# Kernel tuning notes

Measured on AMD Instinct MI355X. Metric: run time of the kernel, lower is better.

The kernel has to match this reference:

```python
import jax, jax.numpy as jnp
import numpy as np

N_NODES = 100000
N_EDGES = 1600000
D_IN = 256
D_OUT = 128


def setup_inputs() -> dict:
    key = jax.random.key(0)
    k1, k2, k3, k4, k5 = jax.random.split(key, 5)
    features = jax.random.normal(k1, (N_NODES, D_IN), dtype=jnp.float32)
    # Xavier-uniform init for weight [in, out]
    limit = float(np.sqrt(6.0 / (D_IN + D_OUT)))
    weight = jax.random.uniform(k2, (D_IN, D_OUT), dtype=jnp.float32, minval=-limit, maxval=limit)
    edge_rows = jax.random.randint(k3, (N_EDGES,), 0, N_NODES, dtype=jnp.int32)
    edge_cols = jax.random.randint(k4, (N_EDGES,), 0, N_NODES, dtype=jnp.int32)
    edge_vals = jax.random.uniform(k5, (N_EDGES,), dtype=jnp.float32)
    return {
        "features": features,
        "weight": weight,
        "edge_rows": edge_rows,
        "edge_cols": edge_cols,
        "edge_vals": edge_vals,
    }


def reference(features, weight, edge_rows, edge_cols, edge_vals):
    # support = X @ W : [N, D_OUT]
    support = features @ weight
    # SpMM with COO adjacency: out[i] = sum_{e: row[e]==i} vals[e] * support[col[e]]
    gathered = edge_vals[:, None] * support[edge_cols]        # [E, D_OUT]
    output = jax.ops.segment_sum(gathered, edge_rows, num_segments=N_NODES)
    # active=True -> fused ReLU
    return jax.nn.relu(output)
```

## Files before the change

kernel.cpp:

```cpp
#include <hip/hip_runtime.h>

#define N_NODES 100000
#define N_EDGES 1600000
#define D_IN    256
#define D_OUT   128

typedef __attribute__((ext_vector_type(8))) short short8;
typedef __attribute__((ext_vector_type(4))) float floatx4;

static __device__ __forceinline__ ushort f2bf(float f) {
    union { float f; unsigned u; } v; v.f = f;
    unsigned r = v.u + 0x7fffu + ((v.u >> 16) & 1u);
    return (ushort)(r >> 16);
}

__global__ __launch_bounds__(256) void gcn_gemm_mfma(
    const float* __restrict__ X,
    const float* __restrict__ W,
    ushort* __restrict__ supp)
{
    __shared__ ushort wp[32 * 128 * 8];

    const int tid  = threadIdx.x;
    const int lane = tid & 63;
    const int wid  = tid >> 6;
    const int node0 = blockIdx.x * 128;

#pragma unroll
    for (int i = 0; i < 16; ++i) {
        const int p   = i * 256 + tid;
        const int kg  = p >> 7;
        const int col = p & 127;
        const float* wsrc = W + (size_t)(kg * 8) * D_OUT + col;
        short8 v;
#pragma unroll
        for (int ki = 0; ki < 8; ++ki)
            v[ki] = (short)f2bf(wsrc[(size_t)ki * D_OUT]);
        *(short8*)&wp[(size_t)p * 8] = v;
    }
    __syncthreads();

    const int r0    = node0 + wid * 32;
    const int g     = lane >> 4;
    const int arow0 = r0 + (lane & 15);
    const int arow1 = arow0 + 16;
    const int crow0 = arow0 < N_NODES - 1 ? arow0 : N_NODES - 1;
    const int crow1 = arow1 < N_NODES - 1 ? arow1 : N_NODES - 1;

    const float* xp0 = X + (size_t)crow0 * D_IN + g * 8;
    const float* xp1 = X + (size_t)crow1 * D_IN + g * 8;

    floatx4 acc[2][8];
#pragma unroll
    for (int t = 0; t < 2; ++t)
#pragma unroll
        for (int n = 0; n < 8; ++n)
            acc[t][n] = (floatx4){0.f, 0.f, 0.f, 0.f};

#pragma unroll
    for (int ks = 0; ks < 8; ++ks) {
        const float4 u0 = *(const float4*)(xp0 + ks * 32);
        const float4 u1 = *(const float4*)(xp0 + ks * 32 + 4);
        const float4 u2 = *(const float4*)(xp1 + ks * 32);
        const float4 u3 = *(const float4*)(xp1 + ks * 32 + 4);
        short8 a0, a1;
        a0[0] = (short)f2bf(u0.x); a0[1] = (short)f2bf(u0.y);
        a0[2] = (short)f2bf(u0.z); a0[3] = (short)f2bf(u0.w);
        a0[4] = (short)f2bf(u1.x); a0[5] = (short)f2bf(u1.y);
        a0[6] = (short)f2bf(u1.z); a0[7] = (short)f2bf(u1.w);
        a1[0] = (short)f2bf(u2.x); a1[1] = (short)f2bf(u2.y);
        a1[2] = (short)f2bf(u2.z); a1[3] = (short)f2bf(u2.w);
        a1[4] = (short)f2bf(u3.x); a1[5] = (short)f2bf(u3.y);
        a1[6] = (short)f2bf(u3.z); a1[7] = (short)f2bf(u3.w);

        const int kg = ks * 4 + g;
#pragma unroll
        for (int n = 0; n < 8; ++n) {
            const short8 b = *(const short8*)&wp[(size_t)((kg << 7) + n * 16 + (lane & 15)) * 8];
            acc[0][n] = __builtin_amdgcn_mfma_f32_16x16x32_bf16(a0, b, acc[0][n], 0, 0, 0);
            acc[1][n] = __builtin_amdgcn_mfma_f32_16x16x32_bf16(a1, b, acc[1][n], 0, 0, 0);
        }
    }

#pragma unroll
    for (int t = 0; t < 2; ++t) {
        const int rbase = r0 + t * 16 + (lane >> 4) * 4;
#pragma unroll
        for (int n = 0; n < 8; ++n) {
            const int col = n * 16 + (lane & 15);
#pragma unroll
            for (int i = 0; i < 4; ++i) {
                const int row = rbase + i;
                if (row < N_NODES)
                    supp[(size_t)row * D_OUT + col] = f2bf(acc[t][n][i]);
            }
        }
    }
}

__global__ __launch_bounds__(256) void gcn_hist_kernel(
    const int* __restrict__ rows, int* __restrict__ counts)
{
    int e = blockIdx.x * 256 + threadIdx.x;
    if (e < N_EDGES) atomicAdd(&counts[rows[e]], 1);
}

__global__ __launch_bounds__(256) void gcn_scan1_kernel(
    const int* __restrict__ counts, int* __restrict__ off, int* __restrict__ bsums)
{
    __shared__ int t[256];
    const int tid = threadIdx.x;
    const int i0 = blockIdx.x * 1024 + tid * 4;

    int c0 = 0, c1 = 0, c2 = 0, c3 = 0;
    if (i0 + 3 < N_NODES) {
        int4 v = *(const int4*)&counts[i0];
        c0 = v.x; c1 = v.y; c2 = v.z; c3 = v.w;
    } else {
        if (i0 + 0 < N_NODES) c0 = counts[i0 + 0];
        if (i0 + 1 < N_NODES) c1 = counts[i0 + 1];
        if (i0 + 2 < N_NODES) c2 = counts[i0 + 2];
        if (i0 + 3 < N_NODES) c3 = counts[i0 + 3];
    }
    const int s = c0 + c1 + c2 + c3;
    t[tid] = s;
    __syncthreads();

    for (int d = 1; d < 256; d <<= 1) {
        int x = t[tid];
        int add = (tid >= d) ? t[tid - d] : 0;
        __syncthreads();
        t[tid] = x + add;
        __syncthreads();
    }
    const int excl = t[tid] - s;
    if (tid == 255) bsums[blockIdx.x] = t[255];

    const int e0 = excl;
    const int e1 = e0 + c0;
    const int e2 = e1 + c1;
    const int e3 = e2 + c2;
    if (i0 + 0 < N_NODES) off[i0 + 0] = e0;
    if (i0 + 1 < N_NODES) off[i0 + 1] = e1;
    if (i0 + 2 < N_NODES) off[i0 + 2] = e2;
    if (i0 + 3 < N_NODES) off[i0 + 3] = e3;
}

__global__ __launch_bounds__(128) void gcn_scan2_kernel(int* __restrict__ bsums, int nb)
{
    __shared__ int t[128];
    const int tid = threadIdx.x;
    const int v = (tid < nb) ? bsums[tid] : 0;
    t[tid] = v;
    __syncthreads();
    for (int d = 1; d < 128; d <<= 1) {
        int x = t[tid];
        int add = (tid >= d) ? t[tid - d] : 0;
        __syncthreads();
        t[tid] = x + add;
        __syncthreads();
    }
    if (tid < nb) bsums[tid] = t[tid] - v;
}

__global__ __launch_bounds__(256) void gcn_scan3_kernel(
    const int* __restrict__ bsums, int* __restrict__ off, int* __restrict__ cursor)
{
    int i = blockIdx.x * 256 + threadIdx.x;
    if (i < N_NODES) {
        int o = off[i] + bsums[i >> 10];
        off[i] = o;
        cursor[i] = o;
    }
}

__global__ __launch_bounds__(256) void gcn_scatter_kernel(
    const int* __restrict__ rows, const int* __restrict__ cols,
    const float* __restrict__ vals, int* __restrict__ cursor,
    int2* __restrict__ edges)
{
    int e = blockIdx.x * 256 + threadIdx.x;
    if (e < N_EDGES) {
        int pos = atomicAdd(&cursor[rows[e]], 1);
        edges[pos] = make_int2(cols[e], __float_as_int(vals[e]));
    }
}

__global__ __launch_bounds__(256) void gcn_aggregate_kernel(
    const int* __restrict__ off, const int* __restrict__ ends,
    const int2* __restrict__ edges, const unsigned* __restrict__ supp2,
    float* __restrict__ out)
{
    const int node = blockIdx.x * 4 + (threadIdx.x >> 6);
    if (node >= N_NODES) return;
    const int lane = threadIdx.x & 63;

    const int start = off[node];
    const int end   = ends[node];

    float accx = 0.f, accy = 0.f;

    for (int base = start; base < end; base += 64) {
        int m = end - base;
        if (m > 64) m = 64;
        int2 e = edges[base + (lane < m ? lane : 0)];
        for (int j = 0; j < m; ++j) {
            const int      col = __shfl(e.x, j);
            const float    v   = __int_as_float(__shfl(e.y, j));
            const unsigned s   = supp2[(size_t)col * 64 + lane];
            accx = fmaf(v, __uint_as_float(s << 16), accx);
            accy = fmaf(v, __uint_as_float(s & 0xffff0000u), accy);
        }
    }

    float2 o;
    o.x = accx > 0.f ? accx : 0.f;
    o.y = accy > 0.f ? accy : 0.f;
    ((float2*)out)[(size_t)node * 64 + lane] = o;
}

extern "C" void kernel_launch(void* const* d_in, const int* in_sizes, int n_in,
                              void* d_out, int out_size, void* d_ws, size_t ws_size,
                              hipStream_t stream)
{
    const float* X    = (const float*)d_in[0];
    const float* W    = (const float*)d_in[1];
    const int*   rows = (const int*)  d_in[2];
    const int*   cols = (const int*)  d_in[3];
    const float* vals = (const float*)d_in[4];
    float* out = (float*)d_out;

    char* ws = (char*)d_ws;
    size_t p = 0;
    ushort* supp   = (ushort*)(ws + p); p += (size_t)N_NODES * D_OUT * 2;
    int*    counts = (int*)   (ws + p); p += (size_t)N_NODES * 4;
    int*    off    = (int*)   (ws + p); p += (size_t)N_NODES * 4;
    int*    cursor = (int*)   (ws + p); p += (size_t)N_NODES * 4;
    int*    bsums  = (int*)   (ws + p); p += 512;
    int2*   edges  = (int2*)  (ws + p); p += (size_t)N_EDGES * 8;
    (void)ws_size;

    const int NB = (N_NODES + 1023) / 1024;

    gcn_gemm_mfma<<<(N_NODES + 127) / 128, 256, 0, stream>>>(X, W, supp);

    (void)hipMemsetAsync(counts, 0, (size_t)N_NODES * 4, stream);
    gcn_hist_kernel<<<(N_EDGES + 255) / 256, 256, 0, stream>>>(rows, counts);
    gcn_scan1_kernel<<<NB, 256, 0, stream>>>(counts, off, bsums);
    gcn_scan2_kernel<<<1, 128, 0, stream>>>(bsums, NB);
    gcn_scan3_kernel<<<(N_NODES + 255) / 256, 256, 0, stream>>>(bsums, off, cursor);
    gcn_scatter_kernel<<<(N_EDGES + 255) / 256, 256, 0, stream>>>(rows, cols, vals, cursor, edges);

    gcn_aggregate_kernel<<<(N_NODES + 3) / 4, 256, 0, stream>>>(
        off, cursor, edges, (const unsigned*)supp, out);
}
```

Measured before the change: 480.4 us.

## Bucket edges by 128-row groups and aggregate with shared-memory atomics

Result: slower. 1.645 ms (+242.5%).

```diff
diff --git a/kernel.cpp b/kernel.cpp
--- a/kernel.cpp
+++ b/kernel.cpp
@@ -4,6 +4,11 @@
 #define N_EDGES 1600000
 #define D_IN    256
 #define D_OUT   128
+
+#define BROWS    128
+#define NBUCKETS ((N_NODES + BROWS - 1) / BROWS)
+#define EPB      4096
+#define NPART    ((N_EDGES + EPB - 1) / EPB)
 
 typedef __attribute__((ext_vector_type(8))) short short8;
 typedef __attribute__((ext_vector_type(4))) float floatx4;
@@ -98,30 +103,40 @@
     }
 }
 
-__global__ __launch_bounds__(256) void gcn_hist_kernel(
-    const int* __restrict__ rows, int* __restrict__ counts)
-{
-    int e = blockIdx.x * 256 + threadIdx.x;
-    if (e < N_EDGES) atomicAdd(&counts[rows[e]], 1);
-}
-
-__global__ __launch_bounds__(256) void gcn_scan1_kernel(
-    const int* __restrict__ counts, int* __restrict__ off, int* __restrict__ bsums)
+__global__ __launch_bounds__(256) void gcn_bcount(
+    const int* __restrict__ rows, int* __restrict__ bcount)
+{
+    __shared__ int h[NBUCKETS];
+    const int tid = threadIdx.x;
+    for (int i = tid; i < NBUCKETS; i += 256) h[i] = 0;
+    __syncthreads();
+
+    const int e0 = blockIdx.x * EPB;
+#pragma unroll
+    for (int i = 0; i < EPB / 256; ++i) {
+        const int e = e0 + i * 256 + tid;
+        if (e < N_EDGES) atomicAdd(&h[rows[e] >> 7], 1);
+    }
+    __syncthreads();
+
+    for (int i = tid; i < NBUCKETS; i += 256) {
+        const int c = h[i];
+        if (c) atomicAdd(&bcount[i], c);
+    }
+}
+
+__global__ __launch_bounds__(256) void gcn_bscan(
+    const int* __restrict__ bcount, int* __restrict__ boff, int* __restrict__ gcursor)
 {
     __shared__ int t[256];
     const int tid = threadIdx.x;
-    const int i0 = blockIdx.x * 1024 + tid * 4;
+    const int i0 = tid * 4;
 
     int c0 = 0, c1 = 0, c2 = 0, c3 = 0;
-    if (i0 + 3 < N_NODES) {
-        int4 v = *(const int4*)&counts[i0];
-        c0 = v.x; c1 = v.y; c2 = v.z; c3 = v.w;
-    } else {
-        if (i0 + 0 < N_NODES) c0 = counts[i0 + 0];
-        if (i0 + 1 < N_NODES) c1 = counts[i0 + 1];
-        if (i0 + 2 < N_NODES) c2 = counts[i0 + 2];
-        if (i0 + 3 < N_NODES) c3 = counts[i0 + 3];
-    }
+    if (i0 + 0 < NBUCKETS) c0 = bcount[i0 + 0];
+    if (i0 + 1 < NBUCKETS) c1 = bcount[i0 + 1];
+    if (i0 + 2 < NBUCKETS) c2 = bcount[i0 + 2];
+    if (i0 + 3 < NBUCKETS) c3 = bcount[i0 + 3];
     const int s = c0 + c1 + c2 + c3;
     t[tid] = s;
     __syncthreads();
@@ -134,89 +149,120 @@
         __syncthreads();
     }
     const int excl = t[tid] - s;
-    if (tid == 255) bsums[blockIdx.x] = t[255];
 
     const int e0 = excl;
     const int e1 = e0 + c0;
     const int e2 = e1 + c1;
     const int e3 = e2 + c2;
-    if (i0 + 0 < N_NODES) off[i0 + 0] = e0;
-    if (i0 + 1 < N_NODES) off[i0 + 1] = e1;
-    if (i0 + 2 < N_NODES) off[i0 + 2] = e2;
-    if (i0 + 3 < N_NODES) off[i0 + 3] = e3;
-}
-
-__global__ __launch_bounds__(128) void gcn_scan2_kernel(int* __restrict__ bsums, int nb)
-{
-    __shared__ int t[128];
+    if (i0 + 0 < NBUCKETS) { boff[i0 + 0] = e0; gcursor[i0 + 0] = e0; }
+    if (i0 + 1 < NBUCKETS) { boff[i0 + 1] = e1; gcursor[i0 + 1] = e1; }
+    if (i0 + 2 < NBUCKETS) { boff[i0 + 2] = e2; gcursor[i0 + 2] = e2; }
+    if (i0 + 3 < NBUCKETS) { boff[i0 + 3] = e3; gcursor[i0 + 3] = e3; }
+}
+
+__global__ __launch_bounds__(256) void gcn_bscatter(
+    const int* __restrict__ rows, const int* __restrict__ cols,
+    const float* __restrict__ vals, int* __restrict__ gcursor,
+    int2* __restrict__ edges)
+{
+    __shared__ int h[NBUCKETS];
     const int tid = threadIdx.x;
-    const int v = (tid < nb) ? bsums[tid] : 0;
-    t[tid] = v;
-    __syncthreads();
-    for (int d = 1; d < 128; d <<= 1) {
-        int x = t[tid];
-        int add = (tid >= d) ? t[tid - d] : 0;
-        __syncthreads();
-        t[tid] = x + add;
-        __syncthreads();
-    }
-    if (tid < nb) bsums[tid] = t[tid] - v;
-}
-
-__global__ __launch_bounds__(256) void gcn_scan3_kernel(
-    const int* __restrict__ bsums, int* __restrict__ off, int* __restrict__ cursor)
-{
-    int i = blockIdx.x * 256 + threadIdx.x;
-    if (i < N_NODES) {
-        int o = off[i] + bsums[i >> 10];
-        off[i] = o;
-        cursor[i] = o;
-    }
-}
-
-__global__ __launch_bounds__(256) void gcn_scatter_kernel(
-    const int* __restrict__ rows, const int* __restrict__ cols,
-    const float* __restrict__ vals, int* __restrict__ cursor,
-    int2* __restrict__ edges)
-{
-    int e = blockIdx.x * 256 + threadIdx.x;
-    if (e < N_EDGES) {
-        int pos = atomicAdd(&cursor[rows[e]], 1);
-        edges[pos] = make_int2(cols[e], __float_as_int(vals[e]));
-    }
-}
-
-__global__ __launch_bounds__(256) void gcn_aggregate_kernel(
-    const int* __restrict__ off, const int* __restrict__ ends,
+    for (int i = tid; i < NBUCKETS; i += 256) h[i] = 0;
+    __syncthreads();
+
+    const int e0 = blockIdx.x * EPB;
+    int bk[EPB / 256];
+    int rl[EPB / 256];
+#pragma unroll
+    for (int i = 0; i < EPB / 256; ++i) {
+        const int e = e0 + i * 256 + tid;
+        bk[i] = -1;
+        if (e < N_EDGES) {
+            const int r = rows[e];
+            bk[i] = r >> 7;
+            rl[i] = r & 127;
+            atomicAdd(&h[bk[i]], 1);
+        }
+    }
+    __syncthreads();
+
+    for (int i = tid; i < NBUCKETS; i += 256) {
+        const int c = h[i];
+        h[i] = c ? atomicAdd(&gcursor[i], c) : 0;
+    }
+    __syncthreads();
+
+#pragma unroll
+    for (int i = 0; i < EPB / 256; ++i) {
+        if (bk[i] >= 0) {
+            const int e = e0 + i * 256 + tid;
+            const int pos = atomicAdd(&h[bk[i]], 1);
+            edges[pos] = make_int2((rl[i] << 17) | cols[e], __float_as_int(vals[e]));
+        }
+    }
+}
+
+__global__ __launch_bounds__(256) void gcn_baggregate(
+    const int* __restrict__ boff, const int* __restrict__ bcount,
     const int2* __restrict__ edges, const unsigned* __restrict__ supp2,
     float* __restrict__ out)
 {
-    const int node = blockIdx.x * 4 + (threadIdx.x >> 6);
-    if (node >= N_NODES) return;
-    const int lane = threadIdx.x & 63;
-
-    const int start = off[node];
-    const int end   = ends[node];
-
-    float accx = 0.f, accy = 0.f;
-
-    for (int base = start; base < end; base += 64) {
+    __shared__ float accL[BROWS * 64];
+    __shared__ float accH[BROWS * 64];
+
+    const int tid  = threadIdx.x;
+    const int lane = tid & 63;
+    const int wid  = tid >> 6;
+
+    {
+        float4 z = make_float4(0.f, 0.f, 0.f, 0.f);
+        float4* aL = (float4*)accL;
+        float4* aH = (float4*)accH;
+#pragma unroll
+        for (int i = 0; i < 8; ++i) { aL[i * 256 + tid] = z; aH[i * 256 + tid] = z; }
+    }
+    __syncthreads();
+
+    const int bkt   = blockIdx.x;
+    const int start = boff[bkt];
+    const int end   = start + bcount[bkt];
+
+    for (int base = start + wid * 64; base < end; base += 256) {
         int m = end - base;
         if (m > 64) m = 64;
         int2 e = edges[base + (lane < m ? lane : 0)];
+#pragma unroll 4
         for (int j = 0; j < m; ++j) {
-            const int      col = __shfl(e.x, j);
-            const float    v   = __int_as_float(__shfl(e.y, j));
+            const int   packed = __shfl(e.x, j);
+            const float v      = __int_as_float(__shfl(e.y, j));
+            const int   col    = packed & 0x1ffff;
+            const int   rl     = packed >> 17;
             const unsigned s   = supp2[(size_t)col * 64 + lane];
-            accx = fmaf(v, __uint_as_float(s << 16), accx);
-            accy = fmaf(v, __uint_as_float(s & 0xffff0000u), accy);
-        }
-    }
-
-    float2 o;
-    o.x = accx > 0.f ? accx : 0.f;
-    o.y = accy > 0.f ? accy : 0.f;
-    ((float2*)out)[(size_t)node * 64 + lane] = o;
+            const float lo = __uint_as_float(s << 16);
+            const float hi = __uint_as_float(s & 0xffff0000u);
+            atomicAdd(&accL[rl * 64 + lane], v * lo);
+            atomicAdd(&accH[rl * 64 + lane], v * hi);
+        }
+    }
+    __syncthreads();
+
+    const int node0 = bkt * BROWS;
+    float2* o2 = (float2*)out;
+#pragma unroll
+    for (int i = 0; i < 32; ++i) {
+        const int f  = i * 256 + tid;
+        const int rl = f >> 6;
+        const int c  = f & 63;
+        const int row = node0 + rl;
+        if (row < N_NODES) {
+            const float x = accL[rl * 64 + c];
+            const float y = accH[rl * 64 + c];
+            float2 w;
+            w.x = x > 0.f ? x : 0.f;
+            w.y = y > 0.f ? y : 0.f;
+            o2[(size_t)row * 64 + c] = w;
+        }
+    }
 }
 
 extern "C" void kernel_launch(void* const* d_in, const int* in_sizes, int n_in,
@@ -232,25 +278,21 @@
 
     char* ws = (char*)d_ws;
     size_t p = 0;
-    ushort* supp   = (ushort*)(ws + p); p += (size_t)N_NODES * D_OUT * 2;
-    int*    counts = (int*)   (ws + p); p += (size_t)N_NODES * 4;
-    int*    off    = (int*)   (ws + p); p += (size_t)N_NODES * 4;
-    int*    cursor = (int*)   (ws + p); p += (size_t)N_NODES * 4;
-    int*    bsums  = (int*)   (ws + p); p += 512;
-    int2*   edges  = (int2*)  (ws + p); p += (size_t)N_EDGES * 8;
+    ushort* supp    = (ushort*)(ws + p); p += (size_t)N_NODES * D_OUT * 2;
+    int*    bcount  = (int*)   (ws + p); p += (size_t)NBUCKETS * 4;
+    int*    boff    = (int*)   (ws + p); p += (size_t)NBUCKETS * 4;
+    int*    gcursor = (int*)   (ws + p); p += (size_t)NBUCKETS * 4;
+    p = (p + 15) & ~(size_t)15;
+    int2*   edges   = (int2*)  (ws + p); p += (size_t)N_EDGES * 8;
     (void)ws_size;
 
-    const int NB = (N_NODES + 1023) / 1024;
-
     gcn_gemm_mfma<<<(N_NODES + 127) / 128, 256, 0, stream>>>(X, W, supp);
 
-    (void)hipMemsetAsync(counts, 0, (size_t)N_NODES * 4, stream);
-    gcn_hist_kernel<<<(N_EDGES + 255) / 256, 256, 0, stream>>>(rows, counts);
-    gcn_scan1_kernel<<<NB, 256, 0, stream>>>(counts, off, bsums);
-    gcn_scan2_kernel<<<1, 128, 0, stream>>>(bsums, NB);
-    gcn_scan3_kernel<<<(N_NODES + 255) / 256, 256, 0, stream>>>(bsums, off, cursor);
-    gcn_scatter_kernel<<<(N_EDGES + 255) / 256, 256, 0, stream>>>(rows, cols, vals, cursor, edges);
-
-    gcn_aggregate_kernel<<<(N_NODES + 3) / 4, 256, 0, stream>>>(
-        off, cursor, edges, (const unsigned*)supp, out);
-}
+    (void)hipMemsetAsync(bcount, 0, (size_t)NBUCKETS * 4, stream);
+    gcn_bcount<<<NPART, 256, 0, stream>>>(rows, bcount);
+    gcn_bscan<<<1, 256, 0, stream>>>(bcount, boff, gcursor);
+    gcn_bscatter<<<NPART, 256, 0, stream>>>(rows, cols, vals, gcursor, edges);
+
+    gcn_baggregate<<<NBUCKETS, 256, 0, stream>>>(
+        boff, bcount, edges, (const unsigned*)supp, out);
+}
```
